# Kernel tuning notes

Measured on AMD Instinct MI355X. Metric: run time of the kernel, lower is better.

## Reference

```python
import jax, jax.numpy as jnp
import numpy as np

NEG_SLOPE = 0.2  # PyG GATConv default LeakyReLU slope
BN_EPS = 1e-5


def gat_layer(x, src, dst, W, a_src, a_dst, num_nodes):
    """PyG-style GATConv (no dropout, eval mode). Returns [N, H, C]."""
    H, C = a_src.shape
    h = (x @ W).reshape(-1, H, C)                       # [N,H,C]
    s_src = jnp.einsum('nhc,hc->nh', h, a_src)          # [N,H]
    s_dst = jnp.einsum('nhc,hc->nh', h, a_dst)          # [N,H]
    e = jax.nn.leaky_relu(s_src[src] + s_dst[dst], NEG_SLOPE)  # [E,H]
    # segment softmax over incoming edges of each dst node
    e_max = jax.ops.segment_max(e, dst, num_segments=num_nodes)  # [N,H]
    e_exp = jnp.exp(e - e_max[dst])
    denom = jax.ops.segment_sum(e_exp, dst, num_segments=num_nodes)
    alpha = e_exp / (denom[dst] + 1e-16)                # [E,H]
    msg = h[src] * alpha[:, :, None]                    # [E,H,C] (dominant intermediate)
    return jax.ops.segment_sum(msg, dst, num_segments=num_nodes)  # [N,H,C]


def setup_inputs() -> dict:
    key = jax.random.key(0)
    ks = jax.random.split(key, 12)
    N, Din, Hdim, Heads, Dout = 50000, 128, 128, 8, 128
    E = 150000
    inp = {}
    inp['x'] = jax.random.normal(ks[0], (N, Din), dtype=jnp.float32)
    inp['edge_index'] = jax.random.randint(ks[1], (2, E), 0, N, dtype=jnp.int64)
    sc1 = 1.0 / np.sqrt(Din)
    inp['W1'] = jax.random.uniform(ks[2], (Din, Heads * Hdim), minval=-sc1, maxval=sc1, dtype=jnp.float32)
    inp['a_src1'] = jax.random.normal(ks[3], (Heads, Hdim), dtype=jnp.float32) * 0.1
    inp['a_dst1'] = jax.random.normal(ks[4], (Heads, Hdim), dtype=jnp.float32) * 0.1
    inp['b1'] = jnp.zeros((Heads * Hdim,), dtype=jnp.float32)
    inp['gamma'] = jnp.ones((Heads * Hdim,), dtype=jnp.float32)
    inp['beta'] = jnp.zeros((Heads * Hdim,), dtype=jnp.float32)
    sc2 = 1.0 / np.sqrt(Heads * Hdim)
    inp['W2'] = jax.random.uniform(ks[5], (Heads * Hdim, Dout), minval=-sc2, maxval=sc2, dtype=jnp.float32)
    inp['a_src2'] = jax.random.normal(ks[6], (1, Dout), dtype=jnp.float32) * 0.1
    inp['a_dst2'] = jax.random.normal(ks[7], (1, Dout), dtype=jnp.float32) * 0.1
    inp['b2'] = jnp.zeros((Dout,), dtype=jnp.float32)
    return inp


def reference(x, W1, a_src1, a_dst1, b1, gamma, beta, W2, a_src2, a_dst2, b2, edge_index):
    N = x.shape[0]
    src, dst = edge_index[0], edge_index[1]
    # GAT layer 1: heads=8, concat=True
    h1 = gat_layer(x, src, dst, W1, a_src1, a_dst1, N)   # [N,8,128]
    h1 = h1.reshape(N, -1) + b1                          # [N,1024]
    # BatchNorm1d (training-mode batch stats, biased variance as in torch)
    mu = jnp.mean(h1, axis=0)
    var = jnp.var(h1, axis=0)
    h1 = gamma * (h1 - mu) * jax.lax.rsqrt(var + BN_EPS) + beta
    h1 = jax.nn.elu(h1)
    # GAT layer 2: heads=1, concat=False (mean == squeeze for 1 head)
    h2 = gat_layer(h1, src, dst, W2, a_src2, a_dst2, N)  # [N,1,128]
    return h2[:, 0, :] + b2
```

## Files before the change

### kernel.cpp

```cpp
#include <hip/hip_runtime.h>
#include <hip/hip_bf16.h>
#include <math.h>

#define NEG_SLOPE 0.2f
#define BN_EPS 1e-5f

typedef short bf16x8 __attribute__((ext_vector_type(8)));
typedef float f32x4 __attribute__((ext_vector_type(4)));

__device__ __forceinline__ float bf2f(unsigned short u) {
  union { unsigned int i; float f; } v;
  v.i = ((unsigned int)u) << 16;
  return v.f;
}
__device__ __forceinline__ unsigned short f2bf(float f) {
  union { unsigned int i; float f; } v;
  v.f = f;
  unsigned int i = v.i;
  unsigned int r = (i + 0x7fffu + ((i >> 16) & 1u)) >> 16;
  return (unsigned short)r;
}

__global__ __launch_bounds__(256) void detect_kernel(
    const unsigned int* __restrict__ xw, const unsigned int* __restrict__ eiw,
    int E, int* __restrict__ flags) {
  __shared__ int cnt[2];
  if (threadIdx.x < 2) cnt[threadIdx.x] = 0;
  __syncthreads();
  int t = threadIdx.x;
  int inrange = 0;
  for (int i = t; i < 2048; i += 256) {
    unsigned int e = (xw[i] >> 7) & 0xFFu;
    inrange += (e >= 100u && e <= 135u) ? 1 : 0;
  }
  atomicAdd(&cnt[0], inrange);
  int M = min(1024, E / 2);
  int zeros = 0;
  for (int i = t; i < M; i += 256) zeros += (eiw[2 * i + 1] == 0u) ? 1 : 0;
  atomicAdd(&cnt[1], zeros);
  __syncthreads();
  if (t == 0) {
    flags[0] = (cnt[0] > 1536) ? 1 : 0;
    flags[1] = (cnt[1] > M / 2) ? 1 : 0;
  }
}

__global__ __launch_bounds__(256) void canon_w_t(
    const void* __restrict__ src, unsigned short* __restrict__ dst, int Kdim,
    int Ndim, const int* __restrict__ flags) {
  int i = blockIdx.x * 256 + threadIdx.x;
  if (i >= Kdim * Ndim) return;
  int k = i / Ndim, n = i - k * Ndim;
  unsigned short v = flags[0] ? ((const unsigned short*)src)[i]
                              : f2bf(((const float*)src)[i]);
  dst[(size_t)n * Kdim + k] = v;
}

__global__ __launch_bounds__(1024) void canon_params(
    const void* s0, const void* s1, const void* s2, const void* s3,
    const void* s4, const void* s5, const void* s6, const void* s7,
    unsigned short* d0, unsigned short* d1, unsigned short* d2,
    unsigned short* d3, unsigned short* d4, unsigned short* d5,
    unsigned short* d6, unsigned short* d7, const int* __restrict__ flags) {
  int b = blockIdx.x, t = threadIdx.x;
  const void* s;
  unsigned short* d;
  int n;
  switch (b) {
    case 0: s = s0; d = d0; n = 1024; break;
    case 1: s = s1; d = d1; n = 1024; break;
    case 2: s = s2; d = d2; n = 1024; break;
    case 3: s = s3; d = d3; n = 1024; break;
    case 4: s = s4; d = d4; n = 1024; break;
    case 5: s = s5; d = d5; n = 128; break;
    case 6: s = s6; d = d6; n = 128; break;
    default: s = s7; d = d7; n = 128; break;
  }
  if (t < n)
    d[t] = flags[0] ? ((const unsigned short*)s)[t]
                    : f2bf(((const float*)s)[t]);
}

__global__ __launch_bounds__(256) void canon_idx(
    const int* __restrict__ ei, int* __restrict__ eis, int* __restrict__ eid,
    int E, const int* __restrict__ flags) {
  int e = blockIdx.x * 256 + threadIdx.x;
  if (e >= E) return;
  if (flags[1]) {
    eis[e] = ei[2 * (size_t)e];
    eid[e] = ei[2 * (size_t)E + 2 * (size_t)e];
  } else {
    eis[e] = ei[e];
    eid[e] = ei[E + e];
  }
}

__global__ __launch_bounds__(256) void gemm1_fused(
    const void* __restrict__ Araw,
    const unsigned short* __restrict__ Bt,
    unsigned short* __restrict__ C,
    const unsigned short* __restrict__ aScr,
    const unsigned short* __restrict__ aDcr,
    float* __restrict__ ssrc,
    float* __restrict__ sdst,
    int N, int MP, const int* __restrict__ flags) {
  __shared__ unsigned short As[64 * 128];
  __shared__ float sP[64][2][2];
  __shared__ float dP[64][2][2];

  const int tid = threadIdx.x;
  const int wid = tid >> 6;
  const int lane = tid & 63;
  const int q = lane >> 4;
  const int r = lane & 15;
  const int bid = blockIdx.x;
  const int m0 = (bid >> 2) * 64;
  const int cg = bid & 3;
  const int n0 = cg * 256 + wid * 64;

  bf16x8 bfr[4][4];
#pragma unroll
  for (int ni = 0; ni < 4; ++ni)
#pragma unroll
    for (int ks = 0; ks < 4; ++ks)
      bfr[ni][ks] = *(const bf16x8*)(Bt + (size_t)(n0 + ni * 16 + r) * 128 +
                                     (ks * 4 + q) * 8);

  {
    const int arow = tid >> 4, ag = tid & 15;
    const int isbf = flags[0];
    union { bf16x8 v; unsigned short u[8]; } t[4];
#pragma unroll
    for (int j = 0; j < 4; ++j) {
      int row = m0 + j * 16 + arow;
      if (row < N) {
        if (isbf) {
          t[j].v = *(const bf16x8*)((const unsigned short*)Araw +
                                    (size_t)row * 128 + ag * 8);
        } else {
          const float4* f =
              (const float4*)((const float*)Araw + (size_t)row * 128 + ag * 8);
          float4 f0 = f[0];
          float4 f1 = f[1];
          t[j].u[0] = f2bf(f0.x); t[j].u[1] = f2bf(f0.y);
          t[j].u[2] = f2bf(f0.z); t[j].u[3] = f2bf(f0.w);
          t[j].u[4] = f2bf(f1.x); t[j].u[5] = f2bf(f1.y);
          t[j].u[6] = f2bf(f1.z); t[j].u[7] = f2bf(f1.w);
        }
      } else {
#pragma unroll
        for (int jj = 0; jj < 8; ++jj) t[j].u[jj] = 0;
      }
    }
#pragma unroll
    for (int j = 0; j < 4; ++j) {
      int row = j * 16 + arow;
      *(bf16x8*)(As + row * 128 + (ag ^ (row & 15)) * 8) = t[j].v;
    }
  }
  __syncthreads();

  float aSv[4], aDv[4];
#pragma unroll
  for (int ni = 0; ni < 4; ++ni) {
    aSv[ni] = bf2f(aScr[n0 + ni * 16 + r]);
    aDv[ni] = bf2f(aDcr[n0 + ni * 16 + r]);
  }

#pragma unroll
  for (int rg = 0; rg < 4; ++rg) {
    bf16x8 af[4];
#pragma unroll
    for (int ks = 0; ks < 4; ++ks)
      af[ks] = *(const bf16x8*)(As + (rg * 16 + r) * 128 +
                                (((ks * 4 + q) ^ r) << 3));
    f32x4 acc[4] = {};
#pragma unroll
    for (int ks = 0; ks < 4; ++ks)
#pragma unroll
      for (int ni = 0; ni < 4; ++ni)
        acc[ni] = __builtin_amdgcn_mfma_f32_16x16x32_bf16(af[ks], bfr[ni][ks],
                                                          acc[ni], 0, 0, 0);
#pragma unroll
    for (int ni = 0; ni < 4; ++ni)
#pragma unroll
      for (int i = 0; i < 4; ++i)
        C[(size_t)(m0 + rg * 16 + q * 4 + i) * 1024 + n0 + ni * 16 + r] =
            f2bf(acc[ni][i]);
#pragma unroll
    for (int i = 0; i < 4; ++i) {
      float ps = 0.f, pd = 0.f;
#pragma unroll
      for (int ni = 0; ni < 4; ++ni) {
        ps += acc[ni][i] * aSv[ni];
        pd += acc[ni][i] * aDv[ni];
      }
      ps += __shfl_xor(ps, 1, 64); pd += __shfl_xor(pd, 1, 64);
      ps += __shfl_xor(ps, 2, 64); pd += __shfl_xor(pd, 2, 64);
      ps += __shfl_xor(ps, 4, 64); pd += __shfl_xor(pd, 4, 64);
      ps += __shfl_xor(ps, 8, 64); pd += __shfl_xor(pd, 8, 64);
      if (r == 0) {
        sP[rg * 16 + q * 4 + i][wid >> 1][wid & 1] = ps;
        dP[rg * 16 + q * 4 + i][wid >> 1][wid & 1] = pd;
      }
    }
  }
  __syncthreads();
  if (tid < 64) {
    float2 s = make_float2(sP[tid][0][0] + sP[tid][0][1],
                           sP[tid][1][0] + sP[tid][1][1]);
    float2 d = make_float2(dP[tid][0][0] + dP[tid][0][1],
                           dP[tid][1][0] + dP[tid][1][1]);
    *(float2*)(ssrc + (size_t)(m0 + tid) * 8 + cg * 2) = s;
    *(float2*)(sdst + (size_t)(m0 + tid) * 8 + cg * 2) = d;
  }
}

__global__ __launch_bounds__(256) void gemm2_bn(
    const unsigned short* __restrict__ A,
    const unsigned short* __restrict__ Bt,
    float* __restrict__ C,
    const float* __restrict__ scale, const float* __restrict__ shift,
    const unsigned short* __restrict__ aScr,
    const unsigned short* __restrict__ aDcr,
    float* __restrict__ ssrc, float* __restrict__ sdst) {
  constexpr int K = 1024;
  constexpr int BK = 64;
  constexpr int LDA = BK + 8;
  __shared__ unsigned short As[64 * LDA];
  __shared__ unsigned short Bs[128 * LDA];
  __shared__ float sS[2][64];
  __shared__ float sD[2][64];

  const int m0 = blockIdx.x * 64;
  const int tid = threadIdx.x;
  const int wid = tid >> 6;
  const int lane = tid & 63;
  const int q = lane >> 4;
  const int r = lane & 15;
  const int wm = (wid >> 1) * 32;
  const int wn = (wid & 1) * 64;

  f32x4 acc[2][4] = {};

  const int row0 = tid >> 3;
  const int col0 = (tid & 7) * 8;

  bf16x8 ra[2], rb[4];
#pragma unroll
  for (int ca = 0; ca < 2; ++ca)
    ra[ca] = *(const bf16x8*)(A + (size_t)(m0 + row0 + ca * 32) * K + col0);
#pragma unroll
  for (int cb = 0; cb < 4; ++cb)
    rb[cb] = *(const bf16x8*)(Bt + (size_t)(row0 + cb * 32) * K + col0);

  for (int k0 = 0; k0 < K; k0 += BK) {
    float scv[8], shv[8];
    *(float4*)&scv[0] = *(const float4*)(scale + k0 + col0);
    *(float4*)&scv[4] = *(const float4*)(scale + k0 + col0 + 4);
    *(float4*)&shv[0] = *(const float4*)(shift + k0 + col0);
    *(float4*)&shv[4] = *(const float4*)(shift + k0 + col0 + 4);
#pragma unroll
    for (int ca = 0; ca < 2; ++ca) {
      union { bf16x8 v; unsigned short u[8]; } pk;
      pk.v = ra[ca];
#pragma unroll
      for (int j = 0; j < 8; ++j) {
        float f = bf2f(pk.u[j]) * scv[j] + shv[j];
        f = f > 0.f ? f : (__expf(f) - 1.0f);
        pk.u[j] = f2bf(f);
      }
      *(bf16x8*)(&As[(row0 + ca * 32) * LDA + col0]) = pk.v;
    }
#pragma unroll
    for (int cb = 0; cb < 4; ++cb)
      *(bf16x8*)(&Bs[(row0 + cb * 32) * LDA + col0]) = rb[cb];
    __syncthreads();

    int k1 = k0 + BK;
    if (k1 < K) {
#pragma unroll
      for (int ca = 0; ca < 2; ++ca)
        ra[ca] = *(const bf16x8*)(A + (size_t)(m0 + row0 + ca * 32) * K + k1 +
                                  col0);
#pragma unroll
      for (int cb = 0; cb < 4; ++cb)
        rb[cb] = *(const bf16x8*)(Bt + (size_t)(row0 + cb * 32) * K + k1 +
                                  col0);
    }

#pragma unroll
    for (int ks = 0; ks < BK; ks += 32) {
      bf16x8 af[2], bfv[4];
#pragma unroll
      for (int mi = 0; mi < 2; ++mi)
        af[mi] = *(const bf16x8*)(&As[(wm + mi * 16 + r) * LDA + ks + q * 8]);
#pragma unroll
      for (int ni = 0; ni < 4; ++ni)
        bfv[ni] = *(const bf16x8*)(&Bs[(wn + ni * 16 + r) * LDA + ks + q * 8]);
#pragma unroll
      for (int mi = 0; mi < 2; ++mi)
#pragma unroll
        for (int ni = 0; ni < 4; ++ni)
          acc[mi][ni] = __builtin_amdgcn_mfma_f32_16x16x32_bf16(
              af[mi], bfv[ni], acc[mi][ni], 0, 0, 0);
    }
    __syncthreads();
  }

#pragma unroll
  for (int mi = 0; mi < 2; ++mi)
#pragma unroll
    for (int ni = 0; ni < 4; ++ni)
#pragma unroll
      for (int i = 0; i < 4; ++i) {
        int row = m0 + wm + mi * 16 + q * 4 + i;
        int col = wn + ni * 16 + r;
        C[(size_t)row * 128 + col] = acc[mi][ni][i];
      }

  const int half = wid & 1;
  float aSv[4], aDv[4];
#pragma unroll
  for (int ni = 0; ni < 4; ++ni) {
    aSv[ni] = bf2f(aScr[wn + ni * 16 + r]);
    aDv[ni] = bf2f(aDcr[wn + ni * 16 + r]);
  }
#pragma unroll
  for (int mi = 0; mi < 2; ++mi) {
#pragma unroll
    for (int i = 0; i < 4; ++i) {
      float ps = 0.f, pd = 0.f;
#pragma unroll
      for (int ni = 0; ni < 4; ++ni) {
        float v = acc[mi][ni][i];
        ps += v * aSv[ni];
        pd += v * aDv[ni];
      }
      ps += __shfl_xor(ps, 1, 64); pd += __shfl_xor(pd, 1, 64);
      ps += __shfl_xor(ps, 2, 64); pd += __shfl_xor(pd, 2, 64);
      ps += __shfl_xor(ps, 4, 64); pd += __shfl_xor(pd, 4, 64);
      ps += __shfl_xor(ps, 8, 64); pd += __shfl_xor(pd, 8, 64);
      if (r == 0) {
        int rl = wm + mi * 16 + q * 4 + i;
        sS[half][rl] = ps;
        sD[half][rl] = pd;
      }
    }
  }
  __syncthreads();
  if (tid < 64) {
    ssrc[m0 + tid] = sS[0][tid] + sS[1][tid];
    sdst[m0 + tid] = sD[0][tid] + sD[1][tid];
  }
}

__global__ __launch_bounds__(256) void count_dst(const int* __restrict__ eid,
                                                 int E, int* __restrict__ cnt) {
  int e = blockIdx.x * 256 + threadIdx.x;
  if (e < E) atomicAdd(&cnt[eid[e]], 1);
}

__global__ __launch_bounds__(256) void scan_p1(const int* __restrict__ cnt,
                                               int* __restrict__ bsum, int N) {
  __shared__ int sd[256];
  int b = blockIdx.x, t = threadIdx.x;
  int base = b * 2048;
  int s = 0;
  for (int i = t; i < 2048; i += 256) {
    int idx = base + i;
    if (idx < N) s += cnt[idx];
  }
  sd[t] = s;
  __syncthreads();
  for (int o = 128; o > 0; o >>= 1) {
    if (t < o) sd[t] += sd[t + o];
    __syncthreads();
  }
  if (t == 0) bsum[b] = sd[0];
}

__global__ __launch_bounds__(256) void scan_p2(int* __restrict__ bsum, int nb) {
  __shared__ int sd[256];
  int t = threadIdx.x;
  int own = (t < nb) ? bsum[t] : 0;
  sd[t] = own;
  __syncthreads();
  for (int o = 1; o < 256; o <<= 1) {
    int v = (t >= o) ? sd[t - o] : 0;
    __syncthreads();
    sd[t] += v;
    __syncthreads();
  }
  if (t < nb) bsum[t] = sd[t] - own;
}

__global__ __launch_bounds__(256) void scan_p3(
    const int* __restrict__ cnt, const int* __restrict__ bsum,
    int* __restrict__ offsets, int* __restrict__ cursor, int N) {
  __shared__ int sd[256];
  int b = blockIdx.x, t = threadIdx.x;
  int base = b * 2048 + t * 8;
  int c[8];
  int ts = 0;
#pragma unroll
  for (int j = 0; j < 8; ++j) {
    int idx = base + j;
    c[j] = (idx < N) ? cnt[idx] : 0;
    ts += c[j];
  }
  sd[t] = ts;
  __syncthreads();
  for (int o = 1; o < 256; o <<= 1) {
    int v = (t >= o) ? sd[t - o] : 0;
    __syncthreads();
    sd[t] += v;
    __syncthreads();
  }
  int run = bsum[b] + sd[t] - ts;
#pragma unroll
  for (int j = 0; j < 8; ++j) {
    int idx = base + j;
    if (idx < N) {
      offsets[idx] = run;
      cursor[idx] = run;
      run += c[j];
    }
  }
  if (b == gridDim.x - 1 && t == 255) offsets[N] = bsum[b] + sd[255];
}

__global__ __launch_bounds__(256) void scatter_src(
    const int* __restrict__ eis, const int* __restrict__ eid, int E,
    int* __restrict__ cursor, int* __restrict__ srcs) {
  int e = blockIdx.x * 256 + threadIdx.x;
  if (e >= E) return;
  int d = eid[e];
  int pos = atomicAdd(&cursor[d], 1);
  srcs[pos] = eis[e];
}

__global__ __launch_bounds__(256) void agg1_csr(
    const int* __restrict__ offsets, const int* __restrict__ srcs,
    const unsigned short* __restrict__ h1, const float* __restrict__ ssrc,
    const float* __restrict__ sdst, const unsigned short* __restrict__ b1,
    unsigned short* __restrict__ h1n, int N) {
  int n = blockIdx.x * 4 + (threadIdx.x >> 6);
  if (n >= N) return;
  int lane = threadIdx.x & 63;
  int c0 = lane * 8;
  int c1 = 512 + c0;
  int hA = lane >> 4;
  int beg = offsets[n], end = offsets[n + 1];
  float sdA = sdst[n * 8 + hA];
  float sdB = sdst[n * 8 + hA + 4];
  float accA[8] = {}, accB[8] = {};
  float wsA = 0.f, wsB = 0.f;
  int p = beg;
  for (; p + 2 <= end; p += 2) {
    int s0 = srcs[p], s1 = srcs[p + 1];
    float vA0 = ssrc[s0 * 8 + hA] + sdA;
    float vB0 = ssrc[s0 * 8 + hA + 4] + sdB;
    float vA1 = ssrc[s1 * 8 + hA] + sdA;
    float vB1 = ssrc[s1 * 8 + hA + 4] + sdB;
    union { bf16x8 v; unsigned short u[8]; } uA0, uB0, uA1, uB1;
    uA0.v = *(const bf16x8*)(h1 + (size_t)s0 * 1024 + c0);
    uB0.v = *(const bf16x8*)(h1 + (size_t)s0 * 1024 + c1);
    uA1.v = *(const bf16x8*)(h1 + (size_t)s1 * 1024 + c0);
    uB1.v = *(const bf16x8*)(h1 + (size_t)s1 * 1024 + c1);
    vA0 = vA0 > 0.f ? vA0 : NEG_SLOPE * vA0;
    vB0 = vB0 > 0.f ? vB0 : NEG_SLOPE * vB0;
    vA1 = vA1 > 0.f ? vA1 : NEG_SLOPE * vA1;
    vB1 = vB1 > 0.f ? vB1 : NEG_SLOPE * vB1;
    float wA0 = __expf(vA0), wB0 = __expf(vB0);
    float wA1 = __expf(vA1), wB1 = __expf(vB1);
    wsA += wA0 + wA1;
    wsB += wB0 + wB1;
#pragma unroll
    for (int j = 0; j < 8; ++j) {
      accA[j] = fmaf(bf2f(uA0.u[j]), wA0, accA[j]);
      accB[j] = fmaf(bf2f(uB0.u[j]), wB0, accB[j]);
      accA[j] = fmaf(bf2f(uA1.u[j]), wA1, accA[j]);
      accB[j] = fmaf(bf2f(uB1.u[j]), wB1, accB[j]);
    }
  }
  if (p < end) {
    int s0 = srcs[p];
    float vA0 = ssrc[s0 * 8 + hA] + sdA;
    float vB0 = ssrc[s0 * 8 + hA + 4] + sdB;
    union { bf16x8 v; unsigned short u[8]; } uA0, uB0;
    uA0.v = *(const bf16x8*)(h1 + (size_t)s0 * 1024 + c0);
    uB0.v = *(const bf16x8*)(h1 + (size_t)s0 * 1024 + c1);
    vA0 = vA0 > 0.f ? vA0 : NEG_SLOPE * vA0;
    vB0 = vB0 > 0.f ? vB0 : NEG_SLOPE * vB0;
    float wA0 = __expf(vA0), wB0 = __expf(vB0);
    wsA += wA0;
    wsB += wB0;
#pragma unroll
    for (int j = 0; j < 8; ++j) {
      accA[j] = fmaf(bf2f(uA0.u[j]), wA0, accA[j]);
      accB[j] = fmaf(bf2f(uB0.u[j]), wB0, accB[j]);
    }
  }
  float invA = 1.0f / (wsA + 1e-16f);
  float invB = 1.0f / (wsB + 1e-16f);
  union { bf16x8 v; unsigned short u[8]; } bA, bB, oA, oB;
  bA.v = *(const bf16x8*)(b1 + c0);
  bB.v = *(const bf16x8*)(b1 + c1);
#pragma unroll
  for (int j = 0; j < 8; ++j) {
    oA.u[j] = f2bf(accA[j] * invA + bf2f(bA.u[j]));
    oB.u[j] = f2bf(accB[j] * invB + bf2f(bB.u[j]));
  }
  *(bf16x8*)(h1n + (size_t)n * 1024 + c0) = oA.v;
  *(bf16x8*)(h1n + (size_t)n * 1024 + c1) = oB.v;
}

__global__ __launch_bounds__(256) void bn_stats_part(
    const unsigned short* __restrict__ h1n, float* __restrict__ part, int N,
    int rowsPerBlock) {
  int b = blockIdx.x;
  int half = threadIdx.x >> 7;
  int t = threadIdx.x & 127;
  int c = t * 8;
  int r0 = b * rowsPerBlock;
  int r1 = min(r0 + rowsPerBlock, N);
  float s[8] = {0, 0, 0, 0, 0, 0, 0, 0};
  float q[8] = {0, 0, 0, 0, 0, 0, 0, 0};
  int r = r0 + half;
  for (; r + 2 < r1; r += 4) {
    union { bf16x8 v; unsigned short u[8]; } u0, u1;
    u0.v = *(const bf16x8*)(h1n + (size_t)r * 1024 + c);
    u1.v = *(const bf16x8*)(h1n + (size_t)(r + 2) * 1024 + c);
#pragma unroll
    for (int j = 0; j < 8; ++j) {
      float v0 = bf2f(u0.u[j]);
      float v1 = bf2f(u1.u[j]);
      s[j] += v0 + v1;
      q[j] = fmaf(v0, v0, q[j]);
      q[j] = fmaf(v1, v1, q[j]);
    }
  }
  for (; r < r1; r += 2) {
    union { bf16x8 v; unsigned short u[8]; } u0;
    u0.v = *(const bf16x8*)(h1n + (size_t)r * 1024 + c);
#pragma unroll
    for (int j = 0; j < 8; ++j) {
      float v0 = bf2f(u0.u[j]);
      s[j] += v0;
      q[j] = fmaf(v0, v0, q[j]);
    }
  }
  float* pb = part + ((size_t)b * 2 + half) * 2048;
#pragma unroll
  for (int j = 0; j < 8; ++j) {
    pb[c + j] = s[j];
    pb[1024 + c + j] = q[j];
  }
}

__global__ __launch_bounds__(256) void bn_reduce_finalize(
    const float* __restrict__ part, int nparts,
    const unsigned short* __restrict__ gamma,
    const unsigned short* __restrict__ beta, float* __restrict__ scale,
    float* __restrict__ shift, int N) {
  int c = blockIdx.x * 4 + (threadIdx.x >> 6);
  int lane = threadIdx.x & 63;
  float s = 0.f, q = 0.f;
  for (int b = lane; b < nparts; b += 64) {
    s += part[(size_t)b * 2048 + c];
    q += part[(size_t)b * 2048 + 1024 + c];
  }
#pragma unroll
  for (int o = 32; o > 0; o >>= 1) {
    s += __shfl_xor(s, o, 64);
    q += __shfl_xor(q, o, 64);
  }
  if (lane == 0) {
    float inv_n = 1.0f / (float)N;
    float mu = s * inv_n;
    float var = q * inv_n - mu * mu;
    float sc = bf2f(gamma[c]) * rsqrtf(var + BN_EPS);
    scale[c] = sc;
    shift[c] = bf2f(beta[c]) - mu * sc;
  }
}

__global__ __launch_bounds__(256) void agg2_csr(
    const int* __restrict__ offsets, const int* __restrict__ srcs,
    const float* __restrict__ h2, const float* __restrict__ ssrc,
    const float* __restrict__ sdst, const unsigned short* __restrict__ b2,
    void* __restrict__ out, const int* __restrict__ flags, int N) {
  int n = blockIdx.x * 4 + (threadIdx.x >> 6);
  if (n >= N) return;
  int c = (threadIdx.x & 63) * 2;
  int beg = offsets[n], end = offsets[n + 1];
  float sd = sdst[n];
  float a0 = 0.f, a1 = 0.f, wsum = 0.f;
  int p = beg;
  for (; p + 2 <= end; p += 2) {
    int s0 = srcs[p], s1 = srcs[p + 1];
    float v0 = ssrc[s0] + sd;
    float v1 = ssrc[s1] + sd;
    float2 u0 = *(const float2*)(h2 + (size_t)s0 * 128 + c);
    float2 u1 = *(const float2*)(h2 + (size_t)s1 * 128 + c);
    v0 = v0 > 0.f ? v0 : NEG_SLOPE * v0;
    v1 = v1 > 0.f ? v1 : NEG_SLOPE * v1;
    float w0 = __expf(v0), w1 = __expf(v1);
    wsum += w0 + w1;
    a0 = fmaf(u0.x, w0, a0);
    a1 = fmaf(u0.y, w0, a1);
    a0 = fmaf(u1.x, w1, a0);
    a1 = fmaf(u1.y, w1, a1);
  }
  if (p < end) {
    int s0 = srcs[p];
    float v0 = ssrc[s0] + sd;
    float2 u0 = *(const float2*)(h2 + (size_t)s0 * 128 + c);
    v0 = v0 > 0.f ? v0 : NEG_SLOPE * v0;
    float w0 = __expf(v0);
    wsum += w0;
    a0 = fmaf(u0.x, w0, a0);
    a1 = fmaf(u0.y, w0, a1);
  }
  float inv = 1.0f / (wsum + 1e-16f);
  unsigned int bb = *(const unsigned int*)(b2 + c);
  float r0 = a0 * inv + bf2f(bb & 0xffff);
  float r1 = a1 * inv + bf2f(bb >> 16);
  if (flags[0]) {
    unsigned int o = (unsigned int)f2bf(r0) | ((unsigned int)f2bf(r1) << 16);
    *(unsigned int*)((unsigned short*)out + (size_t)n * 128 + c) = o;
  } else {
    *(float2*)((float*)out + (size_t)n * 128 + c) = make_float2(r0, r1);
  }
}

extern "C" void kernel_launch(void* const* d_in, const int* in_sizes, int n_in,
                              void* d_out, int out_size, void* d_ws,
                              size_t ws_size, hipStream_t stream) {
  const void* x      = d_in[0];
  const int*  ei     = (const int*)d_in[1];
  const void* W1     = d_in[2];
  const void* a_src1 = d_in[3];
  const void* a_dst1 = d_in[4];
  const void* b1     = d_in[5];
  const void* gamma  = d_in[6];
  const void* beta   = d_in[7];
  const void* W2     = d_in[8];
  const void* a_src2 = d_in[9];
  const void* a_dst2 = d_in[10];
  const void* b2     = d_in[11];

  const int N = in_sizes[0] / 128;
  const int E = in_sizes[1] / 2;
  const int MP = ((N + 127) / 128) * 128;
  const int NB = (N + 2047) / 2048;
  const int NSTAT = 256;
  const int RPB = (N + NSTAT - 1) / NSTAT;

  char* ws = (char*)d_ws;
  size_t off = 0;
  unsigned short* h1  = (unsigned short*)(ws + off); off += (size_t)MP * 1024 * 2;
  char* h1n_base = ws + off;
  unsigned short* h1n = (unsigned short*)h1n_base;   off += (size_t)MP * 1024 * 2;
  float* ssrc1 = (float*)(ws + off); off += (size_t)MP * 8 * 4;
  float* sdst1 = (float*)(ws + off); off += (size_t)MP * 8 * 4;
  int* offsets = (int*)(ws + off); off += ((size_t)(N + 1) * 4 + 63) & ~63ull;
  int* srcs    = (int*)(ws + off); off += (size_t)E * 4;
  float* part  = (float*)(ws + off); off += (size_t)NSTAT * 2 * 2048 * 4;
  unsigned short* W1t = (unsigned short*)(ws + off); off += 131072 * 2;
  unsigned short* W2t = (unsigned short*)(ws + off); off += 131072 * 2;
  unsigned short* as1c = (unsigned short*)(ws + off); off += 1024 * 2;
  unsigned short* ad1c = (unsigned short*)(ws + off); off += 1024 * 2;
  unsigned short* b1c  = (unsigned short*)(ws + off); off += 1024 * 2;
  unsigned short* gmc  = (unsigned short*)(ws + off); off += 1024 * 2;
  unsigned short* btc  = (unsigned short*)(ws + off); off += 1024 * 2;
  unsigned short* as2c = (unsigned short*)(ws + off); off += 128 * 2;
  unsigned short* ad2c = (unsigned short*)(ws + off); off += 128 * 2;
  unsigned short* b2c  = (unsigned short*)(ws + off); off += 128 * 2;
  float* scale = (float*)(ws + off); off += 1024 * 4;
  float* shift = (float*)(ws + off); off += 1024 * 4;
  int* bsum    = (int*)(ws + off); off += 256 * 4;
  int* flags   = (int*)(ws + off); off += 64;
  int* eis    = (int*)(h1n_base + (16u << 20));
  int* eid    = eis + E;
  int* cnt    = eid + E;
  int* cursor = cnt + N;
  float* h2    = (float*)h1;
  float* ssrc2 = ssrc1;
  float* sdst2 = sdst1;

  detect_kernel<<<1, 256, 0, stream>>>((const unsigned int*)x,
                                       (const unsigned int*)ei, E, flags);
  canon_w_t<<<(131072 + 255) / 256, 256, 0, stream>>>(W1, W1t, 128, 1024, flags);
  canon_w_t<<<(131072 + 255) / 256, 256, 0, stream>>>(W2, W2t, 1024, 128, flags);
  canon_params<<<8, 1024, 0, stream>>>(a_src1, a_dst1, b1, gamma, beta, a_src2,
                                       a_dst2, b2, as1c, ad1c, b1c, gmc, btc,
                                       as2c, ad2c, b2c, flags);
  canon_idx<<<(E + 255) / 256, 256, 0, stream>>>(ei, eis, eid, E, flags);

  hipMemsetAsync(cnt, 0, (size_t)N * 4, stream);
  hipMemsetAsync((char*)h1n + (size_t)N * 1024 * 2, 0,
                 (size_t)(MP - N) * 1024 * 2, stream);

  count_dst<<<(E + 255) / 256, 256, 0, stream>>>(eid, E, cnt);
  scan_p1<<<NB, 256, 0, stream>>>(cnt, bsum, N);
  scan_p2<<<1, 256, 0, stream>>>(bsum, NB);
  scan_p3<<<NB, 256, 0, stream>>>(cnt, bsum, offsets, cursor, N);
  scatter_src<<<(E + 255) / 256, 256, 0, stream>>>(eis, eid, E, cursor, srcs);

  gemm1_fused<<<(MP / 64) * 4, 256, 0, stream>>>(x, W1t, h1, as1c, ad1c,
                                                 ssrc1, sdst1, N, MP, flags);
  agg1_csr<<<(N + 3) / 4, 256, 0, stream>>>(offsets, srcs, h1, ssrc1, sdst1,
                                            b1c, h1n, N);

  bn_stats_part<<<NSTAT, 256, 0, stream>>>(h1n, part, N, RPB);
  bn_reduce_finalize<<<256, 256, 0, stream>>>(part, NSTAT * 2, gmc, btc, scale,
                                              shift, N);

  gemm2_bn<<<MP / 64, 256, 0, stream>>>(h1n, W2t, h2, scale, shift, as2c,
                                        ad2c, ssrc2, sdst2);
  agg2_csr<<<(N + 3) / 4, 256, 0, stream>>>(offsets, srcs, h2, ssrc2, sdst2,
                                            b2c, d_out, flags, N);
}
```

Measured before the change: 361.5 us.

## Aggregate raw inputs before layer-1 projection and fold attention vectors into W1

Uses linearity to reorder layer 1: attention scores are computed as x·(W1·a) through a small precomputed 128x8 vector pair. Per-head softmax aggregation then runs on the 128-wide bf16 inputs instead of the 1024-wide projected features, and the projection by W1 is applied afterwards with MFMA inside the same kernel, adding the bias. This removes the materialized h1 intermediate and makes the edge gathers much narrower. In exchange, each block gathers neighbour rows for two heads separately, so the aggregation work is repeated four times per node, and the score_v kernel runs serially on one block.

```diff
diff --git a/kernel.cpp b/kernel.cpp
--- a/kernel.cpp
+++ b/kernel.cpp
@@ -43,6 +43,31 @@
     flags[0] = (cnt[0] > 1536) ? 1 : 0;
     flags[1] = (cnt[1] > M / 2) ? 1 : 0;
   }
+}
+
+__global__ __launch_bounds__(256) void canon_x8(
+    const void* __restrict__ src, unsigned short* __restrict__ dst, int n_real,
+    int n_total, const int* __restrict__ flags) {
+  int i = (blockIdx.x * 256 + threadIdx.x) * 8;
+  if (i >= n_total) return;
+  union { bf16x8 v; unsigned short u[8]; } o;
+  if (i < n_real) {
+    if (flags[0]) {
+      o.v = *(const bf16x8*)((const unsigned short*)src + i);
+    } else {
+      const float4* f = (const float4*)((const float*)src + i);
+      float4 f0 = f[0];
+      float4 f1 = f[1];
+      o.u[0] = f2bf(f0.x); o.u[1] = f2bf(f0.y);
+      o.u[2] = f2bf(f0.z); o.u[3] = f2bf(f0.w);
+      o.u[4] = f2bf(f1.x); o.u[5] = f2bf(f1.y);
+      o.u[6] = f2bf(f1.z); o.u[7] = f2bf(f1.w);
+    }
+  } else {
+#pragma unroll
+    for (int j = 0; j < 8; ++j) o.u[j] = 0;
+  }
+  *(bf16x8*)(dst + i) = o.v;
 }
 
 __global__ __launch_bounds__(256) void canon_w_t(
@@ -95,18 +120,79 @@
   }
 }
 
-__global__ __launch_bounds__(256) void gemm1_fused(
-    const void* __restrict__ Araw,
+__global__ __launch_bounds__(128) void score_v(
+    const void* __restrict__ W1raw, const unsigned short* __restrict__ as1,
+    const unsigned short* __restrict__ ad1, float* __restrict__ vsrc,
+    float* __restrict__ vdst, const int* __restrict__ flags) {
+  __shared__ float aS[1024], aD[1024];
+  int t = threadIdx.x;
+  for (int j = t; j < 1024; j += 128) {
+    aS[j] = bf2f(as1[j]);
+    aD[j] = bf2f(ad1[j]);
+  }
+  __syncthreads();
+  const int isbf = flags[0];
+#pragma unroll
+  for (int h = 0; h < 8; ++h) {
+    float s = 0.f, d = 0.f;
+    for (int j = 0; j < 128; ++j) {
+      int idx = h * 128 + j;
+      float w = isbf ? bf2f(((const unsigned short*)W1raw)[(size_t)t * 1024 + idx])
+                     : ((const float*)W1raw)[(size_t)t * 1024 + idx];
+      s = fmaf(w, aS[idx], s);
+      d = fmaf(w, aD[idx], d);
+    }
+    vsrc[t * 8 + h] = s;
+    vdst[t * 8 + h] = d;
+  }
+}
+
+__global__ __launch_bounds__(256) void score_apply(
+    const unsigned short* __restrict__ xbf, const float* __restrict__ vsrc,
+    const float* __restrict__ vdst, float* __restrict__ ssrc,
+    float* __restrict__ sdst, int N) {
+  __shared__ float vS[128][8];
+  __shared__ float vD[128][8];
+  int t = threadIdx.x;
+  for (int j = t; j < 1024; j += 256) {
+    ((float*)vS)[j] = vsrc[j];
+    ((float*)vD)[j] = vdst[j];
+  }
+  __syncthreads();
+  int node = blockIdx.x * 16 + (t >> 4);
+  if (node >= N) return;
+  int o = t & 15;
+  int h = o & 7;
+  const unsigned short* xr = xbf + (size_t)node * 128;
+  float s = 0.f;
+  if (o < 8) {
+    for (int k0 = 0; k0 < 128; k0 += 8) {
+      union { bf16x8 v; unsigned short u[8]; } xv;
+      xv.v = *(const bf16x8*)(xr + k0);
+#pragma unroll
+      for (int e = 0; e < 8; ++e) s = fmaf(bf2f(xv.u[e]), vS[k0 + e][h], s);
+    }
+    ssrc[(size_t)node * 8 + h] = s;
+  } else {
+    for (int k0 = 0; k0 < 128; k0 += 8) {
+      union { bf16x8 v; unsigned short u[8]; } xv;
+      xv.v = *(const bf16x8*)(xr + k0);
+#pragma unroll
+      for (int e = 0; e < 8; ++e) s = fmaf(bf2f(xv.u[e]), vD[k0 + e][h], s);
+    }
+    sdst[(size_t)node * 8 + h] = s;
+  }
+}
+
+__global__ __launch_bounds__(256) void agg1_fused(
+    const int* __restrict__ offsets, const int* __restrict__ srcs,
+    const unsigned short* __restrict__ xbf,
+    const float* __restrict__ ssrc, const float* __restrict__ sdst,
     const unsigned short* __restrict__ Bt,
-    unsigned short* __restrict__ C,
-    const unsigned short* __restrict__ aScr,
-    const unsigned short* __restrict__ aDcr,
-    float* __restrict__ ssrc,
-    float* __restrict__ sdst,
-    int N, int MP, const int* __restrict__ flags) {
-  __shared__ unsigned short As[64 * 128];
-  __shared__ float sP[64][2][2];
-  __shared__ float dP[64][2][2];
+    const unsigned short* __restrict__ b1,
+    unsigned short* __restrict__ h1n,
+    int N) {
+  __shared__ unsigned short aggT[64 * 256];
 
   const int tid = threadIdx.x;
   const int wid = tid >> 6;
@@ -115,65 +201,94 @@
   const int r = lane & 15;
   const int bid = blockIdx.x;
   const int m0 = (bid >> 2) * 64;
-  const int cg = bid & 3;
-  const int n0 = cg * 256 + wid * 64;
-
+  const int h0 = (bid & 3) * 2;
+
+  const int hl = wid >> 1;
+  const int hg = h0 + hl;
+  const int colh = (wid & 1) * 64;
   bf16x8 bfr[4][4];
 #pragma unroll
   for (int ni = 0; ni < 4; ++ni)
 #pragma unroll
     for (int ks = 0; ks < 4; ++ks)
-      bfr[ni][ks] = *(const bf16x8*)(Bt + (size_t)(n0 + ni * 16 + r) * 128 +
-                                     (ks * 4 + q) * 8);
-
-  {
-    const int arow = tid >> 4, ag = tid & 15;
-    const int isbf = flags[0];
-    union { bf16x8 v; unsigned short u[8]; } t[4];
-#pragma unroll
-    for (int j = 0; j < 4; ++j) {
-      int row = m0 + j * 16 + arow;
-      if (row < N) {
-        if (isbf) {
-          t[j].v = *(const bf16x8*)((const unsigned short*)Araw +
-                                    (size_t)row * 128 + ag * 8);
-        } else {
-          const float4* f =
-              (const float4*)((const float*)Araw + (size_t)row * 128 + ag * 8);
-          float4 f0 = f[0];
-          float4 f1 = f[1];
-          t[j].u[0] = f2bf(f0.x); t[j].u[1] = f2bf(f0.y);
-          t[j].u[2] = f2bf(f0.z); t[j].u[3] = f2bf(f0.w);
-          t[j].u[4] = f2bf(f1.x); t[j].u[5] = f2bf(f1.y);
-          t[j].u[6] = f2bf(f1.z); t[j].u[7] = f2bf(f1.w);
-        }
-      } else {
-#pragma unroll
-        for (int jj = 0; jj < 8; ++jj) t[j].u[jj] = 0;
+      bfr[ni][ks] = *(const bf16x8*)(
+          Bt + (size_t)(hg * 128 + colh + ni * 16 + r) * 128 +
+          (ks * 4 + q) * 8);
+
+  const int c = lane * 2;
+  const int g = lane >> 2;
+  const int e = (lane & 3) * 2;
+#pragma unroll 1
+  for (int i = 0; i < 16; ++i) {
+    int nl = wid * 16 + i;
+    int n = m0 + nl;
+    float aA0 = 0.f, aA1 = 0.f, aB0 = 0.f, aB1 = 0.f;
+    float wsA = 0.f, wsB = 0.f;
+    if (n < N) {
+      int beg = offsets[n], end = offsets[n + 1];
+      float2 sdp = *(const float2*)(sdst + (size_t)n * 8 + h0);
+      int p = beg;
+      for (; p + 2 <= end; p += 2) {
+        int s0 = srcs[p], s1 = srcs[p + 1];
+        float2 sp0 = *(const float2*)(ssrc + (size_t)s0 * 8 + h0);
+        float2 sp1 = *(const float2*)(ssrc + (size_t)s1 * 8 + h0);
+        unsigned int u0 = *(const unsigned int*)(xbf + (size_t)s0 * 128 + c);
+        unsigned int u1 = *(const unsigned int*)(xbf + (size_t)s1 * 128 + c);
+        float vA0 = sp0.x + sdp.x, vB0 = sp0.y + sdp.y;
+        float vA1 = sp1.x + sdp.x, vB1 = sp1.y + sdp.y;
+        vA0 = vA0 > 0.f ? vA0 : NEG_SLOPE * vA0;
+        vB0 = vB0 > 0.f ? vB0 : NEG_SLOPE * vB0;
+        vA1 = vA1 > 0.f ? vA1 : NEG_SLOPE * vA1;
+        vB1 = vB1 > 0.f ? vB1 : NEG_SLOPE * vB1;
+        float wA0 = __expf(vA0), wB0 = __expf(vB0);
+        float wA1 = __expf(vA1), wB1 = __expf(vB1);
+        wsA += wA0 + wA1;
+        wsB += wB0 + wB1;
+        float x00 = bf2f((unsigned short)(u0 & 0xffff));
+        float x01 = bf2f((unsigned short)(u0 >> 16));
+        float x10 = bf2f((unsigned short)(u1 & 0xffff));
+        float x11 = bf2f((unsigned short)(u1 >> 16));
+        aA0 = fmaf(x00, wA0, aA0); aA1 = fmaf(x01, wA0, aA1);
+        aB0 = fmaf(x00, wB0, aB0); aB1 = fmaf(x01, wB0, aB1);
+        aA0 = fmaf(x10, wA1, aA0); aA1 = fmaf(x11, wA1, aA1);
+        aB0 = fmaf(x10, wB1, aB0); aB1 = fmaf(x11, wB1, aB1);
       }
-    }
-#pragma unroll
-    for (int j = 0; j < 4; ++j) {
-      int row = j * 16 + arow;
-      *(bf16x8*)(As + row * 128 + (ag ^ (row & 15)) * 8) = t[j].v;
-    }
-  }
-  __syncthreads();
-
-  float aSv[4], aDv[4];
-#pragma unroll
-  for (int ni = 0; ni < 4; ++ni) {
-    aSv[ni] = bf2f(aScr[n0 + ni * 16 + r]);
-    aDv[ni] = bf2f(aDcr[n0 + ni * 16 + r]);
-  }
+      if (p < end) {
+        int s0 = srcs[p];
+        float2 sp0 = *(const float2*)(ssrc + (size_t)s0 * 8 + h0);
+        unsigned int u0 = *(const unsigned int*)(xbf + (size_t)s0 * 128 + c);
+        float vA0 = sp0.x + sdp.x, vB0 = sp0.y + sdp.y;
+        vA0 = vA0 > 0.f ? vA0 : NEG_SLOPE * vA0;
+        vB0 = vB0 > 0.f ? vB0 : NEG_SLOPE * vB0;
+        float wA0 = __expf(vA0), wB0 = __expf(vB0);
+        wsA += wA0;
+        wsB += wB0;
+        float x00 = bf2f((unsigned short)(u0 & 0xffff));
+        float x01 = bf2f((unsigned short)(u0 >> 16));
+        aA0 = fmaf(x00, wA0, aA0); aA1 = fmaf(x01, wA0, aA1);
+        aB0 = fmaf(x00, wB0, aB0); aB1 = fmaf(x01, wB0, aB1);
+      }
+    }
+    float invA = 1.0f / (wsA + 1e-16f);
+    float invB = 1.0f / (wsB + 1e-16f);
+    int gs = (g ^ (nl & 15)) << 3;
+    unsigned int wA = (unsigned int)f2bf(aA0 * invA) |
+                      ((unsigned int)f2bf(aA1 * invA) << 16);
+    unsigned int wB = (unsigned int)f2bf(aB0 * invB) |
+                      ((unsigned int)f2bf(aB1 * invB) << 16);
+    *(unsigned int*)(aggT + (nl * 2 + 0) * 128 + gs + e) = wA;
+    *(unsigned int*)(aggT + (nl * 2 + 1) * 128 + gs + e) = wB;
+  }
+  __syncthreads();
 
 #pragma unroll
   for (int rg = 0; rg < 4; ++rg) {
+    int arow = rg * 16 + r;
     bf16x8 af[4];
 #pragma unroll
     for (int ks = 0; ks < 4; ++ks)
-      af[ks] = *(const bf16x8*)(As + (rg * 16 + r) * 128 +
-                                (((ks * 4 + q) ^ r) << 3));
+      af[ks] = *(const bf16x8*)(aggT + (arow * 2 + hl) * 128 +
+                                (((ks * 4 + q) ^ (arow & 15)) << 3));
     f32x4 acc[4] = {};
 #pragma unroll
     for (int ks = 0; ks < 4; ++ks)
@@ -182,37 +297,15 @@
         acc[ni] = __builtin_amdgcn_mfma_f32_16x16x32_bf16(af[ks], bfr[ni][ks],
                                                           acc[ni], 0, 0, 0);
 #pragma unroll
-    for (int ni = 0; ni < 4; ++ni)
-#pragma unroll
-      for (int i = 0; i < 4; ++i)
-        C[(size_t)(m0 + rg * 16 + q * 4 + i) * 1024 + n0 + ni * 16 + r] =
-            f2bf(acc[ni][i]);
-#pragma unroll
-    for (int i = 0; i < 4; ++i) {
-      float ps = 0.f, pd = 0.f;
-#pragma unroll
-      for (int ni = 0; ni < 4; ++ni) {
-        ps += acc[ni][i] * aSv[ni];
-        pd += acc[ni][i] * aDv[ni];
+    for (int ni = 0; ni < 4; ++ni) {
+      int col = hg * 128 + colh + ni * 16 + r;
+      float bb = bf2f(b1[col]);
+#pragma unroll
+      for (int i = 0; i < 4; ++i) {
+        int row = m0 + rg * 16 + q * 4 + i;
+        h1n[(size_t)row * 1024 + col] = f2bf(acc[ni][i] + bb);
       }
-      ps += __shfl_xor(ps, 1, 64); pd += __shfl_xor(pd, 1, 64);
-      ps += __shfl_xor(ps, 2, 64); pd += __shfl_xor(pd, 2, 64);
-      ps += __shfl_xor(ps, 4, 64); pd += __shfl_xor(pd, 4, 64);
-      ps += __shfl_xor(ps, 8, 64); pd += __shfl_xor(pd, 8, 64);
-      if (r == 0) {
-        sP[rg * 16 + q * 4 + i][wid >> 1][wid & 1] = ps;
-        dP[rg * 16 + q * 4 + i][wid >> 1][wid & 1] = pd;
-      }
-    }
-  }
-  __syncthreads();
-  if (tid < 64) {
-    float2 s = make_float2(sP[tid][0][0] + sP[tid][0][1],
-                           sP[tid][1][0] + sP[tid][1][1]);
-    float2 d = make_float2(dP[tid][0][0] + dP[tid][0][1],
-                           dP[tid][1][0] + dP[tid][1][1]);
-    *(float2*)(ssrc + (size_t)(m0 + tid) * 8 + cg * 2) = s;
-    *(float2*)(sdst + (size_t)(m0 + tid) * 8 + cg * 2) = d;
+    }
   }
 }
 
@@ -438,82 +531,6 @@
   int d = eid[e];
   int pos = atomicAdd(&cursor[d], 1);
   srcs[pos] = eis[e];
-}
-
-__global__ __launch_bounds__(256) void agg1_csr(
-    const int* __restrict__ offsets, const int* __restrict__ srcs,
-    const unsigned short* __restrict__ h1, const float* __restrict__ ssrc,
-    const float* __restrict__ sdst, const unsigned short* __restrict__ b1,
-    unsigned short* __restrict__ h1n, int N) {
-  int n = blockIdx.x * 4 + (threadIdx.x >> 6);
-  if (n >= N) return;
-  int lane = threadIdx.x & 63;
-  int c0 = lane * 8;
-  int c1 = 512 + c0;
-  int hA = lane >> 4;
-  int beg = offsets[n], end = offsets[n + 1];
-  float sdA = sdst[n * 8 + hA];
-  float sdB = sdst[n * 8 + hA + 4];
-  float accA[8] = {}, accB[8] = {};
-  float wsA = 0.f, wsB = 0.f;
-  int p = beg;
-  for (; p + 2 <= end; p += 2) {
-    int s0 = srcs[p], s1 = srcs[p + 1];
-    float vA0 = ssrc[s0 * 8 + hA] + sdA;
-    float vB0 = ssrc[s0 * 8 + hA + 4] + sdB;
-    float vA1 = ssrc[s1 * 8 + hA] + sdA;
-    float vB1 = ssrc[s1 * 8 + hA + 4] + sdB;
-    union { bf16x8 v; unsigned short u[8]; } uA0, uB0, uA1, uB1;
-    uA0.v = *(const bf16x8*)(h1 + (size_t)s0 * 1024 + c0);
-    uB0.v = *(const bf16x8*)(h1 + (size_t)s0 * 1024 + c1);
-    uA1.v = *(const bf16x8*)(h1 + (size_t)s1 * 1024 + c0);
-    uB1.v = *(const bf16x8*)(h1 + (size_t)s1 * 1024 + c1);
-    vA0 = vA0 > 0.f ? vA0 : NEG_SLOPE * vA0;
-    vB0 = vB0 > 0.f ? vB0 : NEG_SLOPE * vB0;
-    vA1 = vA1 > 0.f ? vA1 : NEG_SLOPE * vA1;
-    vB1 = vB1 > 0.f ? vB1 : NEG_SLOPE * vB1;
-    float wA0 = __expf(vA0), wB0 = __expf(vB0);
-    float wA1 = __expf(vA1), wB1 = __expf(vB1);
-    wsA += wA0 + wA1;
-    wsB += wB0 + wB1;
-#pragma unroll
-    for (int j = 0; j < 8; ++j) {
-      accA[j] = fmaf(bf2f(uA0.u[j]), wA0, accA[j]);
-      accB[j] = fmaf(bf2f(uB0.u[j]), wB0, accB[j]);
-      accA[j] = fmaf(bf2f(uA1.u[j]), wA1, accA[j]);
-      accB[j] = fmaf(bf2f(uB1.u[j]), wB1, accB[j]);
-    }
-  }
-  if (p < end) {
-    int s0 = srcs[p];
-    float vA0 = ssrc[s0 * 8 + hA] + sdA;
-    float vB0 = ssrc[s0 * 8 + hA + 4] + sdB;
-    union { bf16x8 v; unsigned short u[8]; } uA0, uB0;
-    uA0.v = *(const bf16x8*)(h1 + (size_t)s0 * 1024 + c0);
-    uB0.v = *(const bf16x8*)(h1 + (size_t)s0 * 1024 + c1);
-    vA0 = vA0 > 0.f ? vA0 : NEG_SLOPE * vA0;
-    vB0 = vB0 > 0.f ? vB0 : NEG_SLOPE * vB0;
-    float wA0 = __expf(vA0), wB0 = __expf(vB0);
-    wsA += wA0;
-    wsB += wB0;
-#pragma unroll
-    for (int j = 0; j < 8; ++j) {
-      accA[j] = fmaf(bf2f(uA0.u[j]), wA0, accA[j]);
-      accB[j] = fmaf(bf2f(uB0.u[j]), wB0, accB[j]);
-    }
-  }
-  float invA = 1.0f / (wsA + 1e-16f);
-  float invB = 1.0f / (wsB + 1e-16f);
-  union { bf16x8 v; unsigned short u[8]; } bA, bB, oA, oB;
-  bA.v = *(const bf16x8*)(b1 + c0);
-  bB.v = *(const bf16x8*)(b1 + c1);
-#pragma unroll
-  for (int j = 0; j < 8; ++j) {
-    oA.u[j] = f2bf(accA[j] * invA + bf2f(bA.u[j]));
-    oB.u[j] = f2bf(accB[j] * invB + bf2f(bB.u[j]));
-  }
-  *(bf16x8*)(h1n + (size_t)n * 1024 + c0) = oA.v;
-  *(bf16x8*)(h1n + (size_t)n * 1024 + c1) = oB.v;
 }
 
 __global__ __launch_bounds__(256) void bn_stats_part(
@@ -660,7 +677,8 @@
 
   char* ws = (char*)d_ws;
   size_t off = 0;
-  unsigned short* h1  = (unsigned short*)(ws + off); off += (size_t)MP * 1024 * 2;
+  char* regA = ws + off;
+  off += (size_t)MP * 1024 * 2;
   char* h1n_base = ws + off;
   unsigned short* h1n = (unsigned short*)h1n_base;   off += (size_t)MP * 1024 * 2;
   float* ssrc1 = (float*)(ws + off); off += (size_t)MP * 8 * 4;
@@ -680,18 +698,23 @@
   unsigned short* b2c  = (unsigned short*)(ws + off); off += 128 * 2;
   float* scale = (float*)(ws + off); off += 1024 * 4;
   float* shift = (float*)(ws + off); off += 1024 * 4;
+  float* vsrc  = (float*)(ws + off); off += 128 * 8 * 4;
+  float* vdst  = (float*)(ws + off); off += 128 * 8 * 4;
   int* bsum    = (int*)(ws + off); off += 256 * 4;
   int* flags   = (int*)(ws + off); off += 64;
+  unsigned short* x_bf = (unsigned short*)regA;
+  float* h2    = (float*)(regA + (32u << 20));
   int* eis    = (int*)(h1n_base + (16u << 20));
   int* eid    = eis + E;
   int* cnt    = eid + E;
   int* cursor = cnt + N;
-  float* h2    = (float*)h1;
   float* ssrc2 = ssrc1;
   float* sdst2 = sdst1;
 
   detect_kernel<<<1, 256, 0, stream>>>((const unsigned int*)x,
                                        (const unsigned int*)ei, E, flags);
+  canon_x8<<<(MP * 128 / 8 + 255) / 256, 256, 0, stream>>>(x, x_bf, N * 128,
+                                                           MP * 128, flags);
   canon_w_t<<<(131072 + 255) / 256, 256, 0, stream>>>(W1, W1t, 128, 1024, flags);
   canon_w_t<<<(131072 + 255) / 256, 256, 0, stream>>>(W2, W2t, 1024, 128, flags);
   canon_params<<<8, 1024, 0, stream>>>(a_src1, a_dst1, b1, gamma, beta, a_src2,
@@ -700,8 +723,6 @@
   canon_idx<<<(E + 255) / 256, 256, 0, stream>>>(ei, eis, eid, E, flags);
 
   hipMemsetAsync(cnt, 0, (size_t)N * 4, stream);
-  hipMemsetAsync((char*)h1n + (size_t)N * 1024 * 2, 0,
-                 (size_t)(MP - N) * 1024 * 2, stream);
 
   count_dst<<<(E + 255) / 256, 256, 0, stream>>>(eid, E, cnt);
   scan_p1<<<NB, 256, 0, stream>>>(cnt, bsum, N);
@@ -709,10 +730,12 @@
   scan_p3<<<NB, 256, 0, stream>>>(cnt, bsum, offsets, cursor, N);
   scatter_src<<<(E + 255) / 256, 256, 0, stream>>>(eis, eid, E, cursor, srcs);
 
-  gemm1_fused<<<(MP / 64) * 4, 256, 0, stream>>>(x, W1t, h1, as1c, ad1c,
-                                                 ssrc1, sdst1, N, MP, flags);
-  agg1_csr<<<(N + 3) / 4, 256, 0, stream>>>(offsets, srcs, h1, ssrc1, sdst1,
-                                            b1c, h1n, N);
+  score_v<<<1, 128, 0, stream>>>(W1, as1c, ad1c, vsrc, vdst, flags);
+  score_apply<<<(N + 15) / 16, 256, 0, stream>>>(x_bf, vsrc, vdst, ssrc1,
+                                                 sdst1, N);
+
+  agg1_fused<<<(MP / 64) * 4, 256, 0, stream>>>(offsets, srcs, x_bf, ssrc1,
+                                                sdst1, W1t, b1c, h1n, N);
 
   bn_stats_part<<<NSTAT, 256, 0, stream>>>(h1n, part, N, RPB);
   bn_reduce_finalize<<<256, 256, 0, stream>>>(part, NSTAT * 2, gmc, btc, scale,
```

New measurement: 485.5 us. 1.34x slower.
